# Kernel optimization log

Measured on AMD Instinct MI355X. Metric: run time of the kernel, lower is better.

The kernel has to match this reference:

```python
import jax, jax.numpy as jnp
import numpy as np

D = 512
MOMENTUM = 0.99
NEG_INF = -1.0e9


def setup_inputs() -> dict:
    key = jax.random.key(0)
    ks = jax.random.split(key, 16)
    B, Lq, Lk = 16, 1024, 1024
    s = 0.02
    inp = {
        "uncond_q": jax.random.normal(ks[0], (B, D), jnp.float32),
        "q": jax.random.normal(ks[1], (B, Lq, D), jnp.float32),
        "k": jax.random.normal(ks[2], (B, Lk, D), jnp.float32),
        "v": jax.random.normal(ks[3], (B, Lk, D), jnp.float32),
        "src_key_padding_mask": jax.random.randint(ks[4], (B, Lk), 0, 2) > 0,
        "fallback_score": jnp.zeros((1,), jnp.float32),
        # parameters (torch Linear: y = x @ W.T + b)
        "Wv": jax.random.normal(ks[5], (D, D), jnp.float32) * s,
        "bv": jnp.zeros((D,), jnp.float32),
        "Wf": jax.random.normal(ks[6], (D, D), jnp.float32) * s,
        "bf": jnp.zeros((D,), jnp.float32),
        "W1": jax.random.normal(ks[7], (D, D), jnp.float32) * s,
        "b1": jnp.zeros((D,), jnp.float32),
        "W2": jax.random.normal(ks[8], (D // 2, D), jnp.float32) * s,
        "b2": jnp.zeros((D // 2,), jnp.float32),
        "W3": jax.random.normal(ks[9], (1, D // 2), jnp.float32) * s,
        "b3": jnp.zeros((1,), jnp.float32),
    }
    return inp


def _scorer(x, W1, b1, W2, b2, W3, b3):
    h = jax.nn.relu(x @ W1.T + b1)
    h = jax.nn.relu(h @ W2.T + b2)
    return jnp.tanh(h @ W3.T + b3)


def reference(uncond_q, q, k, v, src_key_padding_mask, fallback_score,
              Wv, bv, Wf, bf, W1, b1, W2, b2, W3, b3):
    B, Lq, _ = q.shape
    v_p = v @ Wv.T + bv                                  # [B,Lk,D]
    default_values = (uncond_q @ Wf.T + bf)[:, None, :]  # [B,1,D]

    scores = jnp.einsum('bqd,bkd->bqk', q, k) / jnp.sqrt(jnp.float32(D))

    # EMA fallback-score update (training mode), detached from grads
    bmax = jax.lax.stop_gradient(scores.max())
    bmin = jax.lax.stop_gradient(scores.min())
    fb = MOMENTUM * fallback_score[0] + (1.0 - MOMENTUM) * (bmax + bmin) / 2.0

    scores = jnp.where(src_key_padding_mask[:, None, :], NEG_INF, scores)
    fb_col = jnp.broadcast_to(fb, (B, Lq, 1))
    scores = jnp.concatenate([scores, fb_col], axis=-1)   # [B,Lq,Lk+1]
    weights = jax.nn.softmax(scores, axis=-1)

    v_padded = jnp.concatenate([v_p, default_values], axis=1)  # [B,Lk+1,D]
    out = jnp.einsum('bqk,bkd->bqd', weights, v_padded)

    return (_scorer(out, W1, b1, W2, b2, W3, b3),
            _scorer(default_values, W1, b1, W2, b2, W3, b3))
```

## Files before the change

### kernel.cpp

```cpp
#include <hip/hip_runtime.h>

typedef _Float16 f16;
typedef f16  f16x8 __attribute__((ext_vector_type(8)));
typedef f16  f16x4 __attribute__((ext_vector_type(4)));
typedef __fp16 fp16x2 __attribute__((ext_vector_type(2)));
typedef float f32x4 __attribute__((ext_vector_type(4)));

__device__ __forceinline__ void gld_lds16(const f16* g, void* l) {
  __builtin_amdgcn_global_load_lds((const __attribute__((address_space(1))) void*)g,
                                   (__attribute__((address_space(3))) void*)l,
                                   16, 0, 0);
}

__device__ __forceinline__ f16x8 pack8(float4 a, float4 b) {
  union { f16x8 v; fp16x2 h[4]; } u;
  u.h[0] = __builtin_amdgcn_cvt_pkrtz(a.x, a.y);
  u.h[1] = __builtin_amdgcn_cvt_pkrtz(a.z, a.w);
  u.h[2] = __builtin_amdgcn_cvt_pkrtz(b.x, b.y);
  u.h[3] = __builtin_amdgcn_cvt_pkrtz(b.z, b.w);
  return u.v;
}

enum { EPI_SCORES = 0, EPI_RELU = 2, EPI_OUT = 3, EPI_BIASR = 4 };

template<int EPI, bool XMAP>
__global__ __launch_bounds__(256)
void gemm_bt(const f16* __restrict__ A, const f16* __restrict__ B, void* __restrict__ C,
             int lda, int ldb, int ldc, int K,
             long long sA, long long sB, long long sC,
             const float* __restrict__ bias, float scale,
             float* __restrict__ mmarr, int nmm,
             const float* __restrict__ wfb, const float* __restrict__ dvv,
             int nx, int nbz)
{
  __shared__ __align__(16) f16 As[4][128][32];
  __shared__ __align__(16) f16 Bs[4][128][32];
  const int tid  = threadIdx.x;
  const int lane = tid & 63;
  const int w    = tid >> 6;
  const int wm   = w >> 1, wn = w & 1;

  const int lin = blockIdx.x;
  int bz, bj;
  if constexpr (XMAP) {
    const int xcd = lin & 7, rest = lin >> 3;
    const int grp = rest / nbz;
    bj = rest - grp * nbz;
    bz = xcd + (grp << 3);
  } else {
    bz = lin / nbz; bj = lin - bz * nbz;
  }
  const int m0 = (bj / nx) * 128, n0 = (bj % nx) * 128;
  const f16* Ab = A + (size_t)bz * sA + (size_t)m0 * lda;
  const f16* Bb = B + (size_t)bz * sB + (size_t)n0 * ldb;

  f32x4 acc[4][4] = {};
  const int nsteps = K >> 5;

#define STAGE(bufb, ks)                                                              \
  {                                                                                  \
    const int k0_ = (ks) << 5;                                                       \
    _Pragma("unroll")                                                                \
    for (int i = 0; i < 2; ++i) {                                                    \
      const int ci = i * 256 + tid;                                                  \
      const int r  = ci >> 2;                                                        \
      const int sg = (ci & 3) ^ ((r >> 1) & 3);                                      \
      gld_lds16(Ab + (size_t)r * lda + k0_ + sg * 8,                                 \
                (char*)As + (bufb) + (size_t)(i * 256 + w * 64) * 16);               \
      gld_lds16(Bb + (size_t)r * ldb + k0_ + sg * 8,                                 \
                (char*)Bs + (bufb) + (size_t)(i * 256 + w * 64) * 16);               \
    }                                                                                \
  }

  STAGE(0, 0)
  if (1 < nsteps) STAGE(8192, 1)
  if (2 < nsteps) STAGE(16384, 2)

  const int elemoff = (((lane >> 4) ^ ((lane >> 1) & 3)) << 3);

  int cur = 0;
  for (int t = 0; t < nsteps; ++t) {
    if (t + 2 < nsteps)      asm volatile("s_waitcnt vmcnt(8)" ::: "memory");
    else if (t + 1 < nsteps) asm volatile("s_waitcnt vmcnt(4)" ::: "memory");
    else                     asm volatile("s_waitcnt vmcnt(0)" ::: "memory");
    __builtin_amdgcn_s_barrier();
    __builtin_amdgcn_sched_barrier(0);
    if (t + 3 < nsteps) STAGE(((cur + 3) & 3) * 8192, t + 3)
    f16x8 af[4], bfr[4];
#pragma unroll
    for (int m = 0; m < 4; ++m)
      af[m] = *(const f16x8*)&As[cur][wm * 64 + m * 16 + (lane & 15)][elemoff];
#pragma unroll
    for (int n = 0; n < 4; ++n)
      bfr[n] = *(const f16x8*)&Bs[cur][wn * 64 + n * 16 + (lane & 15)][elemoff];
    __builtin_amdgcn_s_setprio(1);
#pragma unroll
    for (int m = 0; m < 4; ++m)
#pragma unroll
      for (int n = 0; n < 4; ++n)
        acc[m][n] = __builtin_amdgcn_mfma_f32_16x16x32_f16(af[m], bfr[n], acc[m][n], 0, 0, 0);
    __builtin_amdgcn_s_setprio(0);
    cur = (cur + 1) & 3;
  }
#undef STAGE

  const int col_l = lane & 15;
  const int row_l = (lane >> 4) << 2;

  {
    f16* Ch = (f16*)C + (size_t)bz * sC + (size_t)m0 * ldc + n0;
#pragma unroll
    for (int m = 0; m < 4; ++m)
#pragma unroll
      for (int n = 0; n < 4; ++n)
#pragma unroll
        for (int r = 0; r < 4; ++r) {
          const int rr = wm * 64 + m * 16 + row_l + r;
          const int cc = wn * 64 + n * 16 + col_l;
          float val = acc[m][n][r];
          if constexpr (EPI == EPI_RELU) { val += bias[n0 + cc]; val = fmaxf(val, 0.0f); }
          if constexpr (EPI == EPI_BIASR) val += bias[m0 + rr];
          if constexpr (EPI == EPI_OUT)
            val += wfb[bz * 1024 + m0 + rr] * dvv[bz * 512 + n0 + cc];
          Ch[(size_t)rr * ldc + cc] = (f16)val;
        }
  }
  (void)scale; (void)mmarr; (void)nmm;
}

__global__ __launch_bounds__(512, 2)
void gemm256_scores(const float* __restrict__ A, const float* __restrict__ B, f16* __restrict__ C,
                    float scale, float* __restrict__ mmarr)
{
  __shared__ __align__(16) f16 As[3][256][32];
  __shared__ __align__(16) f16 Bs[3][256][32];
  __shared__ float redm[8], redn[8];
  const int tid  = threadIdx.x;
  const int lane = tid & 63;
  const int w    = tid >> 6;
  const int wm   = w >> 2, wn = w & 3;
  const int lin  = blockIdx.x;
  const int xcd = lin & 7, rest = lin >> 3;
  const int bj  = rest & 15;
  const int bz  = xcd + ((rest >> 4) << 3);
  const int m0 = (bj >> 2) * 256, n0 = (bj & 3) * 256;
  const float* Ab = A + (size_t)bz * 524288 + (size_t)m0 * 512;
  const float* Bb = B + (size_t)bz * 524288 + (size_t)n0 * 512;

  const int r0  = tid >> 2;
  const int sg0 = (tid & 3) ^ ((r0 >> 1) & 3);
  const size_t offG = (size_t)r0 * 512 + sg0 * 8;
  f16* const dstA0 = (f16*)As + (size_t)tid * 8;
  f16* const dstB0 = (f16*)Bs + (size_t)tid * 8;

  f32x4 acc[8][4] = {};

#pragma unroll
  for (int s = 0; s < 2; ++s) {
    const int k0 = s << 5;
    float4 a0 = *(const float4*)(Ab + offG + k0);
    float4 a1 = *(const float4*)(Ab + offG + k0 + 4);
    float4 a2 = *(const float4*)(Ab + offG + k0 + 65536);
    float4 a3 = *(const float4*)(Ab + offG + k0 + 65540);
    float4 b0 = *(const float4*)(Bb + offG + k0);
    float4 b1 = *(const float4*)(Bb + offG + k0 + 4);
    float4 b2 = *(const float4*)(Bb + offG + k0 + 65536);
    float4 b3 = *(const float4*)(Bb + offG + k0 + 65540);
    *(f16x8*)(dstA0 + s * 8192)        = pack8(a0, a1);
    *(f16x8*)(dstA0 + s * 8192 + 4096) = pack8(a2, a3);
    *(f16x8*)(dstB0 + s * 8192)        = pack8(b0, b1);
    *(f16x8*)(dstB0 + s * 8192 + 4096) = pack8(b2, b3);
  }
  __syncthreads();

  const int fr = lane & 15;
  const int elemoff = (((lane >> 4) ^ ((lane >> 1) & 3)) << 3);

  int cur = 0;
  for (int t = 0; t < 16; ++t) {
    float4 a0, a1, a2, a3, b0, b1, b2, b3;
    if (t + 2 < 16) {
      const int k0 = (t + 2) << 5;
      a0 = *(const float4*)(Ab + offG + k0);
      a1 = *(const float4*)(Ab + offG + k0 + 4);
      a2 = *(const float4*)(Ab + offG + k0 + 65536);
      a3 = *(const float4*)(Ab + offG + k0 + 65540);
      b0 = *(const float4*)(Bb + offG + k0);
      b1 = *(const float4*)(Bb + offG + k0 + 4);
      b2 = *(const float4*)(Bb + offG + k0 + 65536);
      b3 = *(const float4*)(Bb + offG + k0 + 65540);
    }
    f16x8 af[8], bfr[4];
#pragma unroll
    for (int m = 0; m < 8; ++m)
      af[m] = *(const f16x8*)&As[cur][wm * 128 + m * 16 + fr][elemoff];
#pragma unroll
    for (int n = 0; n < 4; ++n)
      bfr[n] = *(const f16x8*)&Bs[cur][wn * 64 + n * 16 + fr][elemoff];
    __builtin_amdgcn_s_setprio(1);
#pragma unroll
    for (int m = 0; m < 8; ++m)
#pragma unroll
      for (int n = 0; n < 4; ++n)
        acc[m][n] = __builtin_amdgcn_mfma_f32_16x16x32_f16(af[m], bfr[n], acc[m][n], 0, 0, 0);
    __builtin_amdgcn_s_setprio(0);
    if (t + 2 < 16) {
      int wb = cur + 2; if (wb >= 3) wb -= 3;
      *(f16x8*)(dstA0 + wb * 8192)        = pack8(a0, a1);
      *(f16x8*)(dstA0 + wb * 8192 + 4096) = pack8(a2, a3);
      *(f16x8*)(dstB0 + wb * 8192)        = pack8(b0, b1);
      *(f16x8*)(dstB0 + wb * 8192 + 4096) = pack8(b2, b3);
    }
    __syncthreads();
    cur = (cur + 1 == 3) ? 0 : cur + 1;
  }

  const int col_l = lane & 15;
  const int row_l = (lane >> 4) << 2;
  f16* Ch = C + (size_t)bz * 1048576 + (size_t)m0 * 1024 + n0;
  float lmax = -3.402823466e38f, lmin = 3.402823466e38f;
#pragma unroll
  for (int m = 0; m < 8; ++m)
#pragma unroll
    for (int n = 0; n < 4; ++n)
#pragma unroll
      for (int r = 0; r < 4; ++r) {
        float val = acc[m][n][r] * scale;
        lmax = fmaxf(lmax, val); lmin = fminf(lmin, val);
        Ch[(size_t)(wm * 128 + m * 16 + row_l + r) * 1024 + (wn * 64 + n * 16 + col_l)] = (f16)val;
      }
#pragma unroll
  for (int off = 32; off >= 1; off >>= 1) {
    lmax = fmaxf(lmax, __shfl_xor(lmax, off));
    lmin = fminf(lmin, __shfl_xor(lmin, off));
  }
  if (lane == 0) { redm[w] = lmax; redn[w] = lmin; }
  __syncthreads();
  if (tid == 0) {
    float gm = redm[0], gn = redn[0];
#pragma unroll
    for (int i = 1; i < 8; ++i) { gm = fmaxf(gm, redm[i]); gn = fminf(gn, redn[i]); }
    mmarr[lin] = gm; mmarr[256 + lin] = gn;
  }
}

__global__ __launch_bounds__(256)
void gemm_vpt(const f16* __restrict__ A, const float* __restrict__ B, f16* __restrict__ C,
              const float* __restrict__ bias)
{
  __shared__ __align__(16) f16 As[3][128][32];
  __shared__ __align__(16) f16 Bs[3][128][32];
  const int tid  = threadIdx.x;
  const int lane = tid & 63;
  const int w    = tid >> 6;
  const int wm   = w >> 1, wn = w & 1;
  const int lin  = blockIdx.x;
  const int xcd = lin & 7, rest = lin >> 3;
  const int grp = rest >> 5, bj = rest & 31;
  const int bz  = xcd + (grp << 3);
  const int m0 = (bj >> 3) * 128, n0 = (bj & 7) * 128;
  const f16*   Ab = A + (size_t)m0 * 512;
  const float* Bb = B + (size_t)bz * 524288 + (size_t)n0 * 512;

  const int r0  = tid >> 2;
  const int sg0 = (tid & 3) ^ ((r0 >> 1) & 3);
  const size_t offA = (size_t)r0 * 512 + sg0 * 8;
  const size_t offB = (size_t)r0 * 512 + sg0 * 8;
  f16* const dstA0 = (f16*)As + (size_t)tid * 8;
  f16* const dstB0 = (f16*)Bs + (size_t)tid * 8;

  f32x4 acc[4][4] = {};

#pragma unroll
  for (int s = 0; s < 2; ++s) {
    const int k0 = s << 5;
    f16x8  a0 = *(const f16x8*)(Ab + offA + k0);
    f16x8  a1 = *(const f16x8*)(Ab + offA + k0 + 32768);
    float4 b0 = *(const float4*)(Bb + offB + k0);
    float4 b1 = *(const float4*)(Bb + offB + k0 + 4);
    float4 b2 = *(const float4*)(Bb + offB + k0 + 32768);
    float4 b3 = *(const float4*)(Bb + offB + k0 + 32772);
    *(f16x8*)(dstA0 + s * 4096)        = a0;
    *(f16x8*)(dstA0 + s * 4096 + 2048) = a1;
    *(f16x8*)(dstB0 + s * 4096)        = pack8(b0, b1);
    *(f16x8*)(dstB0 + s * 4096 + 2048) = pack8(b2, b3);
  }
  __syncthreads();

  const int fr = lane & 15;
  const int elemoff = (((lane >> 4) ^ ((lane >> 1) & 3)) << 3);

  int cur = 0;
  for (int t = 0; t < 16; ++t) {
    f16x8  a0, a1; float4 b0, b1, b2, b3;
    if (t + 2 < 16) {
      const int k0 = (t + 2) << 5;
      a0 = *(const f16x8*)(Ab + offA + k0);
      a1 = *(const f16x8*)(Ab + offA + k0 + 32768);
      b0 = *(const float4*)(Bb + offB + k0);
      b1 = *(const float4*)(Bb + offB + k0 + 4);
      b2 = *(const float4*)(Bb + offB + k0 + 32768);
      b3 = *(const float4*)(Bb + offB + k0 + 32772);
    }
    f16x8 af[4], bfr[4];
#pragma unroll
    for (int m = 0; m < 4; ++m)
      af[m] = *(const f16x8*)&As[cur][wm * 64 + m * 16 + fr][elemoff];
#pragma unroll
    for (int n = 0; n < 4; ++n)
      bfr[n] = *(const f16x8*)&Bs[cur][wn * 64 + n * 16 + fr][elemoff];
    __builtin_amdgcn_s_setprio(1);
#pragma unroll
    for (int m = 0; m < 4; ++m)
#pragma unroll
      for (int n = 0; n < 4; ++n)
        acc[m][n] = __builtin_amdgcn_mfma_f32_16x16x32_f16(af[m], bfr[n], acc[m][n], 0, 0, 0);
    __builtin_amdgcn_s_setprio(0);
    if (t + 2 < 16) {
      int wb = cur + 2; if (wb >= 3) wb -= 3;
      *(f16x8*)(dstA0 + wb * 4096)        = a0;
      *(f16x8*)(dstA0 + wb * 4096 + 2048) = a1;
      *(f16x8*)(dstB0 + wb * 4096)        = pack8(b0, b1);
      *(f16x8*)(dstB0 + wb * 4096 + 2048) = pack8(b2, b3);
    }
    __syncthreads();
    cur = (cur + 1 == 3) ? 0 : cur + 1;
  }

  const int col_l = lane & 15;
  const int row_l = (lane >> 4) << 2;
  f16* Ch = C + (size_t)bz * 524288 + (size_t)m0 * 1024 + n0;
#pragma unroll
  for (int m = 0; m < 4; ++m)
#pragma unroll
    for (int n = 0; n < 4; ++n)
#pragma unroll
      for (int r = 0; r < 4; ++r) {
        const int rr = wm * 64 + m * 16 + row_l + r;
        const int cc = wn * 64 + n * 16 + col_l;
        Ch[(size_t)rr * 1024 + cc] = (f16)(acc[m][n][r] + bias[m0 + rr]);
      }
}

__global__ __launch_bounds__(256)
void reduce_mm(const float* __restrict__ mmarr, int n,
               const float* __restrict__ fallback, float* __restrict__ fbv,
               const unsigned char* __restrict__ mask, unsigned* __restrict__ mm)
{
  __shared__ float rm[4], rn[4];
  __shared__ int redc[256];
  const int lane = threadIdx.x & 63, w = threadIdx.x >> 6;
  float mx = -3.402823466e38f, mn = 3.402823466e38f;
  for (int i = threadIdx.x; i < n; i += 256) {
    mx = fmaxf(mx, mmarr[i]);
    mn = fminf(mn, mmarr[n + i]);
  }
#pragma unroll
  for (int off = 32; off >= 1; off >>= 1) {
    mx = fmaxf(mx, __shfl_xor(mx, off));
    mn = fminf(mn, __shfl_xor(mn, off));
  }
  if (lane == 0) { rm[w] = mx; rn[w] = mn; }
  int c = 0;
  for (int i = threadIdx.x; i < 16384; i += 256) c += (mask[i] != 0) ? 1 : 0;
  redc[threadIdx.x] = c;
  __syncthreads();
  for (int s = 128; s > 0; s >>= 1) {
    if (threadIdx.x < s) redc[threadIdx.x] += redc[threadIdx.x + s];
    __syncthreads();
  }
  if (threadIdx.x == 0) {
    float gmax = fmaxf(fmaxf(rm[0], rm[1]), fmaxf(rm[2], rm[3]));
    float gmin = fminf(fminf(rn[0], rn[1]), fminf(rn[2], rn[3]));
    fbv[0] = 0.99f * fallback[0] + 0.005f * (gmax + gmin);
    mm[0] = (unsigned)redc[0];
  }
}

__global__ __launch_bounds__(256)
void front_k(const float* __restrict__ wv, const float* __restrict__ w1,
             const float* __restrict__ w2,
             f16* __restrict__ owv, f16* __restrict__ ow1, f16* __restrict__ ow2,
             const float* __restrict__ uq, const float* __restrict__ Wf,
             const float* __restrict__ bfv, float* __restrict__ dv)
{
  const int blk = blockIdx.x;
  if (blk < 640) {
    int i = blk * 256 + threadIdx.x;
    const float* src; f16* dst; int j;
    if (i < 65536)       { src = wv; dst = owv; j = i; }
    else if (i < 131072) { src = w1; dst = ow1; j = i - 65536; }
    else                 { src = w2; dst = ow2; j = i - 131072; }
    float4 x = *(const float4*)(src + (size_t)j * 4);
    f16x4 o = { (f16)x.x, (f16)x.y, (f16)x.z, (f16)x.w };
    *(f16x4*)(dst + (size_t)j * 4) = o;
  } else {
    const int gw   = ((blk - 640) * 256 + threadIdx.x) >> 6;
    const int lane = threadIdx.x & 63;
    const int b = gw >> 9, j = gw & 511;
    const float* x  = uq + (size_t)b * 512;
    const float* wr = Wf + (size_t)j * 512;
    const int o = lane * 8;
    float4 x0 = *(const float4*)(x + o),  x1 = *(const float4*)(x + o + 4);
    float4 w0 = *(const float4*)(wr + o), w1v = *(const float4*)(wr + o + 4);
    float s = x0.x*w0.x + x0.y*w0.y + x0.z*w0.z + x0.w*w0.w
            + x1.x*w1v.x + x1.y*w1v.y + x1.z*w1v.z + x1.w*w1v.w;
#pragma unroll
    for (int off = 32; off >= 1; off >>= 1) s += __shfl_xor(s, off);
    if (lane == 0) dv[gw] = s + bfv[j];
  }
}

__global__ __launch_bounds__(256)
void softmax_rows(const f16* __restrict__ scores, const void* __restrict__ maskp,
                  const float* __restrict__ fbv, const unsigned* __restrict__ mm,
                  f16* __restrict__ Wt, float* __restrict__ wfb)
{
  __shared__ float red[8];
  const int row  = blockIdx.x;
  const int b    = row >> 10;
  const int tid  = threadIdx.x;
  const int lane = tid & 63, w = tid >> 6;
  const float fb = fbv[0];
  const unsigned mode = (mm[0] > 5000u) ? 1u : 0u;
  const f16* s = scores + (size_t)row * 1024;
  const int k0 = tid * 4;
  f16x4 sv = *(const f16x4*)(s + k0);
  float x[4];
  if (mode) {
    const unsigned char* m8 = (const unsigned char*)maskp + b * 1024 + k0;
    x[0] = m8[0] ? -1e9f : (float)sv[0];  x[1] = m8[1] ? -1e9f : (float)sv[1];
    x[2] = m8[2] ? -1e9f : (float)sv[2];  x[3] = m8[3] ? -1e9f : (float)sv[3];
  } else {
    const int* mi = (const int*)maskp + b * 1024 + k0;
    x[0] = mi[0] ? -1e9f : (float)sv[0];  x[1] = mi[1] ? -1e9f : (float)sv[1];
    x[2] = mi[2] ? -1e9f : (float)sv[2];  x[3] = mi[3] ? -1e9f : (float)sv[3];
  }
  float mx = fmaxf(fmaxf(x[0], x[1]), fmaxf(x[2], x[3]));
#pragma unroll
  for (int off = 32; off >= 1; off >>= 1) mx = fmaxf(mx, __shfl_xor(mx, off));
  if (lane == 0) red[w] = mx;
  __syncthreads();
  mx = fmaxf(fmaxf(fmaxf(red[0], red[1]), fmaxf(red[2], red[3])), fb);
  float e0 = expf(x[0] - mx), e1 = expf(x[1] - mx), e2 = expf(x[2] - mx), e3 = expf(x[3] - mx);
  float sum = (e0 + e1) + (e2 + e3);
#pragma unroll
  for (int off = 32; off >= 1; off >>= 1) sum += __shfl_xor(sum, off);
  if (lane == 0) red[4 + w] = sum;
  __syncthreads();
  float efb = expf(fb - mx);
  float Z = ((red[4] + red[5]) + (red[6] + red[7])) + efb;
  float inv = 1.0f / Z;
  f16x4 o = { (f16)(e0 * inv), (f16)(e1 * inv), (f16)(e2 * inv), (f16)(e3 * inv) };
  *(f16x4*)&Wt[(size_t)row * 1024 + k0] = o;
  if (tid == 0) wfb[row] = efb * inv;
}

template<int IN, int ACT>
__global__ __launch_bounds__(256)
void fc_wave(const float* __restrict__ X, const float* __restrict__ W,
             const float* __restrict__ bias, float* __restrict__ Y, int OutN)
{
  const int gw   = (blockIdx.x * 256 + threadIdx.x) >> 6;
  const int lane = threadIdx.x & 63;
  const int b = gw / OutN, j = gw - b * OutN;
  const float* x  = X + (size_t)b * IN;
  const float* wr = W + (size_t)j * IN;
  float s = 0.f;
  if constexpr (IN == 512) {
    const int o = lane * 8;
    float4 x0 = *(const float4*)(x + o),  x1 = *(const float4*)(x + o + 4);
    float4 w0 = *(const float4*)(wr + o), w1 = *(const float4*)(wr + o + 4);
    s = x0.x*w0.x + x0.y*w0.y + x0.z*w0.z + x0.w*w0.w
      + x1.x*w1.x + x1.y*w1.y + x1.z*w1.z + x1.w*w1.w;
  } else {
    const int o = lane * 4;
    float4 x0 = *(const float4*)(x + o);
    float4 w0 = *(const float4*)(wr + o);
    s = x0.x*w0.x + x0.y*w0.y + x0.z*w0.z + x0.w*w0.w;
  }
#pragma unroll
  for (int off = 32; off >= 1; off >>= 1) s += __shfl_xor(s, off);
  if (lane == 0) {
    float val = s + bias[ACT == 2 ? 0 : j];
    if constexpr (ACT == 1) val = fmaxf(val, 0.f);
    if constexpr (ACT == 2) val = tanhf(val);
    Y[gw] = val;
  }
}

__global__ __launch_bounds__(256)
void y_kernel(const f16* __restrict__ h2, const float* __restrict__ W3,
              const float* __restrict__ b3, float* __restrict__ outp)
{
  int row = blockIdx.x * 16 + (threadIdx.x >> 4);
  int l   = threadIdx.x & 15;
  const f16* h = h2 + (size_t)row * 256 + l * 16;
  float s = 0.f;
#pragma unroll
  for (int j = 0; j < 16; ++j) s += (float)h[j] * W3[l * 16 + j];
#pragma unroll
  for (int off = 1; off < 16; off <<= 1) s += __shfl_xor(s, off);
  if (l == 0) outp[row] = tanhf(s + b3[0]);
}

extern "C" void kernel_launch(void* const* d_in, const int* in_sizes, int n_in,
                              void* d_out, int out_size, void* d_ws, size_t ws_size,
                              hipStream_t stream) {
  const float* uq       = (const float*)d_in[0];
  const float* q        = (const float*)d_in[1];
  const float* kk       = (const float*)d_in[2];
  const float* v        = (const float*)d_in[3];
  const void*  mask     = d_in[4];
  const float* fallback = (const float*)d_in[5];
  const float* Wv = (const float*)d_in[6];
  const float* bv = (const float*)d_in[7];
  const float* Wf = (const float*)d_in[8];
  const float* bf = (const float*)d_in[9];
  const float* W1 = (const float*)d_in[10];
  const float* b1 = (const float*)d_in[11];
  const float* W2 = (const float*)d_in[12];
  const float* b2 = (const float*)d_in[13];
  const float* W3 = (const float*)d_in[14];
  const float* b3 = (const float*)d_in[15];
  float* outp = (float*)d_out;

  char* ws = (char*)d_ws;
  const size_t MB = 1ull << 20;
  f16*  scores = (f16*)ws;
  f16*  h1b  = (f16*)ws;
  f16*  h2b  = (f16*)(ws + 16 * MB);
  f16*  vpt  = (f16*)(ws + 32 * MB);
  f16*  outb = (f16*)(ws + 48 * MB);
  f16*  wts  = (f16*)(ws + 64 * MB);
  char* cst  = ws + 112 * MB;
  f16*  Wv16 = (f16*)(cst);
  f16*  W116 = (f16*)(cst + 512 * 1024);
  f16*  W216 = (f16*)(cst + 1024 * 1024);
  float* dv   = (float*)(cst + 1280 * 1024);
  float* wfb  = (float*)(cst + 1312 * 1024);
  float* h1d  = (float*)(cst + 1376 * 1024);
  float* h2d  = (float*)(cst + 1408 * 1024);
  unsigned* mm = (unsigned*)(cst + 1424 * 1024);
  float* fbv   = (float*)(cst + 1428 * 1024);
  float* mmarr = (float*)(cst + 1432 * 1024);

  front_k<<<2688, 256, 0, stream>>>(Wv, W1, W2, Wv16, W116, W216,
                                    uq, Wf, bf, dv);

  gemm256_scores<<<256, 512, 0, stream>>>(q, kk, scores, 0.04419417382415922f, mmarr);

  reduce_mm<<<1, 256, 0, stream>>>(mmarr, 256, fallback, fbv,
                                   (const unsigned char*)mask, mm);

  softmax_rows<<<16384, 256, 0, stream>>>(scores, mask, fbv, mm, wts, wfb);

  gemm_vpt<<<512, 256, 0, stream>>>(Wv16, v, vpt, bv);

  gemm_bt<EPI_OUT, true><<<512, 256, 0, stream>>>(
      wts, vpt, outb, 1024, 1024, 512, 1024,
      1048576LL, 524288LL, 524288LL,
      nullptr, 1.f, nullptr, 0, wfb, dv, 4, 32);

  gemm_bt<EPI_RELU, false><<<512, 256, 0, stream>>>(
      outb, W116, h1b, 512, 512, 512, 512, 0LL, 0LL, 0LL,
      b1, 1.f, nullptr, 0, nullptr, nullptr, 4, 512);

  gemm_bt<EPI_RELU, false><<<256, 256, 0, stream>>>(
      h1b, W216, h2b, 512, 512, 256, 512, 0LL, 0LL, 0LL,
      b2, 1.f, nullptr, 0, nullptr, nullptr, 2, 256);

  y_kernel<<<1024, 256, 0, stream>>>(h2b, W3, b3, outp);

  fc_wave<512, 1><<<2048, 256, 0, stream>>>(dv, W1, b1, h1d, 512);
  fc_wave<512, 1><<<1024, 256, 0, stream>>>(h1d, W2, b2, h2d, 256);
  fc_wave<256, 2><<<4, 256, 0, stream>>>(h2d, W3, b3, outp + 16384, 1);

  (void)in_sizes; (void)n_in; (void)out_size; (void)ws_size;
}
```

Measured before the change: 161.2 us.

## Fuse softmax and V projection into one launch, fold reductions into existing kernels

Merges the row softmax and the V-projection GEMM into a single heterogeneous kernel whose block index selects which role to play. The global min/max reduction is recomputed redundantly in every softmax block, and the mask count moves into an extra block of the front kernel, so the single-block reduce_mm launch goes away. The aim is to cut two kernel launches and serial gaps, and to let the GEMM blocks overlap with softmax blocks. In exchange each softmax block now reads 512 floats and does extra reductions and barriers. The shared-memory footprint becomes the larger GEMM size for all blocks, which may reduce softmax occupancy.

```diff
diff --git a/kernel.cpp b/kernel.cpp
--- a/kernel.cpp
+++ b/kernel.cpp
@@ -29,7 +29,6 @@
              int lda, int ldb, int ldc, int K,
              long long sA, long long sB, long long sC,
              const float* __restrict__ bias, float scale,
-             float* __restrict__ mmarr, int nmm,
              const float* __restrict__ wfb, const float* __restrict__ dvv,
              int nx, int nbz)
 {
@@ -125,7 +124,7 @@
           Ch[(size_t)rr * ldc + cc] = (f16)val;
         }
   }
-  (void)scale; (void)mmarr; (void)nmm;
+  (void)scale;
 }
 
 __global__ __launch_bounds__(512, 2)
@@ -245,135 +244,158 @@
 }
 
 __global__ __launch_bounds__(256)
-void gemm_vpt(const f16* __restrict__ A, const float* __restrict__ B, f16* __restrict__ C,
-              const float* __restrict__ bias)
+void smvp(const f16* __restrict__ scores, const void* __restrict__ maskp,
+          const float* __restrict__ fallback, const float* __restrict__ mmarr,
+          const unsigned* __restrict__ mm,
+          f16* __restrict__ Wt, float* __restrict__ wfb,
+          const f16* __restrict__ Wv16, const float* __restrict__ v,
+          f16* __restrict__ vpt, const float* __restrict__ bv)
 {
-  __shared__ __align__(16) f16 As[3][128][32];
-  __shared__ __align__(16) f16 Bs[3][128][32];
+  __shared__ __align__(16) char smem[49152];
+  const int blk  = blockIdx.x;
   const int tid  = threadIdx.x;
   const int lane = tid & 63;
   const int w    = tid >> 6;
-  const int wm   = w >> 1, wn = w & 1;
-  const int lin  = blockIdx.x;
-  const int xcd = lin & 7, rest = lin >> 3;
-  const int grp = rest >> 5, bj = rest & 31;
-  const int bz  = xcd + (grp << 3);
-  const int m0 = (bj >> 3) * 128, n0 = (bj & 7) * 128;
-  const f16*   Ab = A + (size_t)m0 * 512;
-  const float* Bb = B + (size_t)bz * 524288 + (size_t)n0 * 512;
-
-  const int r0  = tid >> 2;
-  const int sg0 = (tid & 3) ^ ((r0 >> 1) & 3);
-  const size_t offA = (size_t)r0 * 512 + sg0 * 8;
-  const size_t offB = (size_t)r0 * 512 + sg0 * 8;
-  f16* const dstA0 = (f16*)As + (size_t)tid * 8;
-  f16* const dstB0 = (f16*)Bs + (size_t)tid * 8;
-
-  f32x4 acc[4][4] = {};
-
-#pragma unroll
-  for (int s = 0; s < 2; ++s) {
-    const int k0 = s << 5;
-    f16x8  a0 = *(const f16x8*)(Ab + offA + k0);
-    f16x8  a1 = *(const f16x8*)(Ab + offA + k0 + 32768);
-    float4 b0 = *(const float4*)(Bb + offB + k0);
-    float4 b1 = *(const float4*)(Bb + offB + k0 + 4);
-    float4 b2 = *(const float4*)(Bb + offB + k0 + 32768);
-    float4 b3 = *(const float4*)(Bb + offB + k0 + 32772);
-    *(f16x8*)(dstA0 + s * 4096)        = a0;
-    *(f16x8*)(dstA0 + s * 4096 + 2048) = a1;
-    *(f16x8*)(dstB0 + s * 4096)        = pack8(b0, b1);
-    *(f16x8*)(dstB0 + s * 4096 + 2048) = pack8(b2, b3);
-  }
-  __syncthreads();
-
-  const int fr = lane & 15;
-  const int elemoff = (((lane >> 4) ^ ((lane >> 1) & 3)) << 3);
-
-  int cur = 0;
-  for (int t = 0; t < 16; ++t) {
-    f16x8  a0, a1; float4 b0, b1, b2, b3;
-    if (t + 2 < 16) {
-      const int k0 = (t + 2) << 5;
-      a0 = *(const f16x8*)(Ab + offA + k0);
-      a1 = *(const f16x8*)(Ab + offA + k0 + 32768);
-      b0 = *(const float4*)(Bb + offB + k0);
-      b1 = *(const float4*)(Bb + offB + k0 + 4);
-      b2 = *(const float4*)(Bb + offB + k0 + 32768);
-      b3 = *(const float4*)(Bb + offB + k0 + 32772);
-    }
-    f16x8 af[4], bfr[4];
+
+  if (blk < 16384) {
+    float* red = (float*)smem;
+    float mx0 = mmarr[tid];
+    float mn0 = mmarr[256 + tid];
+#pragma unroll
+    for (int off = 32; off >= 1; off >>= 1) {
+      mx0 = fmaxf(mx0, __shfl_xor(mx0, off));
+      mn0 = fminf(mn0, __shfl_xor(mn0, off));
+    }
+    if (lane == 0) { red[w] = mx0; red[4 + w] = mn0; }
+    __syncthreads();
+    const float gmax = fmaxf(fmaxf(red[0], red[1]), fmaxf(red[2], red[3]));
+    const float gmin = fminf(fminf(red[4], red[5]), fminf(red[6], red[7]));
+    const float fb = 0.99f * fallback[0] + 0.005f * (gmax + gmin);
+    const unsigned mode = (mm[0] > 5000u) ? 1u : 0u;
+    __syncthreads();
+    const int row = blk;
+    const int b   = row >> 10;
+    const f16* s = scores + (size_t)row * 1024;
+    const int k0 = tid * 4;
+    f16x4 sv = *(const f16x4*)(s + k0);
+    float x[4];
+    if (mode) {
+      const unsigned char* m8 = (const unsigned char*)maskp + b * 1024 + k0;
+      x[0] = m8[0] ? -1e9f : (float)sv[0];  x[1] = m8[1] ? -1e9f : (float)sv[1];
+      x[2] = m8[2] ? -1e9f : (float)sv[2];  x[3] = m8[3] ? -1e9f : (float)sv[3];
+    } else {
+      const int* mi = (const int*)maskp + b * 1024 + k0;
+      x[0] = mi[0] ? -1e9f : (float)sv[0];  x[1] = mi[1] ? -1e9f : (float)sv[1];
+      x[2] = mi[2] ? -1e9f : (float)sv[2];  x[3] = mi[3] ? -1e9f : (float)sv[3];
+    }
+    float mx = fmaxf(fmaxf(x[0], x[1]), fmaxf(x[2], x[3]));
+#pragma unroll
+    for (int off = 32; off >= 1; off >>= 1) mx = fmaxf(mx, __shfl_xor(mx, off));
+    if (lane == 0) red[w] = mx;
+    __syncthreads();
+    mx = fmaxf(fmaxf(fmaxf(red[0], red[1]), fmaxf(red[2], red[3])), fb);
+    float e0 = expf(x[0] - mx), e1 = expf(x[1] - mx), e2 = expf(x[2] - mx), e3 = expf(x[3] - mx);
+    float sum = (e0 + e1) + (e2 + e3);
+#pragma unroll
+    for (int off = 32; off >= 1; off >>= 1) sum += __shfl_xor(sum, off);
+    if (lane == 0) red[4 + w] = sum;
+    __syncthreads();
+    float efb = expf(fb - mx);
+    float Z = ((red[4] + red[5]) + (red[6] + red[7])) + efb;
+    float inv = 1.0f / Z;
+    f16x4 o = { (f16)(e0 * inv), (f16)(e1 * inv), (f16)(e2 * inv), (f16)(e3 * inv) };
+    *(f16x4*)&Wt[(size_t)row * 1024 + k0] = o;
+    if (tid == 0) wfb[row] = efb * inv;
+  } else {
+    f16* const AsB = (f16*)smem;
+    f16* const BsB = AsB + 12288;
+    const int wm = w >> 1, wn = w & 1;
+    const int lin  = blk - 16384;
+    const int xcd = lin & 7, rest = lin >> 3;
+    const int grp = rest >> 5, bj = rest & 31;
+    const int bz  = xcd + (grp << 3);
+    const int m0 = (bj >> 3) * 128, n0 = (bj & 7) * 128;
+    const f16*   Ab = Wv16 + (size_t)m0 * 512;
+    const float* Bb = v + (size_t)bz * 524288 + (size_t)n0 * 512;
+
+    const int r0  = tid >> 2;
+    const int sg0 = (tid & 3) ^ ((r0 >> 1) & 3);
+    const size_t offA = (size_t)r0 * 512 + sg0 * 8;
+    const size_t offB = (size_t)r0 * 512 + sg0 * 8;
+    f16* const dstA0 = AsB + (size_t)tid * 8;
+    f16* const dstB0 = BsB + (size_t)tid * 8;
+
+    f32x4 acc[4][4] = {};
+
+#pragma unroll
+    for (int s = 0; s < 2; ++s) {
+      const int k0 = s << 5;
+      f16x8  a0 = *(const f16x8*)(Ab + offA + k0);
+      f16x8  a1 = *(const f16x8*)(Ab + offA + k0 + 32768);
+      float4 b0 = *(const float4*)(Bb + offB + k0);
+      float4 b1 = *(const float4*)(Bb + offB + k0 + 4);
+      float4 b2 = *(const float4*)(Bb + offB + k0 + 32768);
+      float4 b3 = *(const float4*)(Bb + offB + k0 + 32772);
+      *(f16x8*)(dstA0 + s * 4096)        = a0;
+      *(f16x8*)(dstA0 + s * 4096 + 2048) = a1;
+      *(f16x8*)(dstB0 + s * 4096)        = pack8(b0, b1);
+      *(f16x8*)(dstB0 + s * 4096 + 2048) = pack8(b2, b3);
+    }
+    __syncthreads();
+
+    const int fr = lane & 15;
+    const int elemoff = (((lane >> 4) ^ ((lane >> 1) & 3)) << 3);
+
+    int cur = 0;
+    for (int t = 0; t < 16; ++t) {
+      f16x8  a0, a1; float4 b0, b1, b2, b3;
+      if (t + 2 < 16) {
+        const int k0 = (t + 2) << 5;
+        a0 = *(const f16x8*)(Ab + offA + k0);
+        a1 = *(const f16x8*)(Ab + offA + k0 + 32768);
+        b0 = *(const float4*)(Bb + offB + k0);
+        b1 = *(const float4*)(Bb + offB + k0 + 4);
+        b2 = *(const float4*)(Bb + offB + k0 + 32768);
+        b3 = *(const float4*)(Bb + offB + k0 + 32772);
+      }
+      f16x8 af[4], bfr[4];
+#pragma unroll
+      for (int m = 0; m < 4; ++m)
+        af[m] = *(const f16x8*)(AsB + cur * 4096 + (wm * 64 + m * 16 + fr) * 32 + elemoff);
+#pragma unroll
+      for (int n = 0; n < 4; ++n)
+        bfr[n] = *(const f16x8*)(BsB + cur * 4096 + (wn * 64 + n * 16 + fr) * 32 + elemoff);
+      __builtin_amdgcn_s_setprio(1);
+#pragma unroll
+      for (int m = 0; m < 4; ++m)
+#pragma unroll
+        for (int n = 0; n < 4; ++n)
+          acc[m][n] = __builtin_amdgcn_mfma_f32_16x16x32_f16(af[m], bfr[n], acc[m][n], 0, 0, 0);
+      __builtin_amdgcn_s_setprio(0);
+      if (t + 2 < 16) {
+        int wb = cur + 2; if (wb >= 3) wb -= 3;
+        *(f16x8*)(dstA0 + wb * 4096)        = a0;
+        *(f16x8*)(dstA0 + wb * 4096 + 2048) = a1;
+        *(f16x8*)(dstB0 + wb * 4096)        = pack8(b0, b1);
+        *(f16x8*)(dstB0 + wb * 4096 + 2048) = pack8(b2, b3);
+      }
+      __syncthreads();
+      cur = (cur + 1 == 3) ? 0 : cur + 1;
+    }
+
+    const int col_l = lane & 15;
+    const int row_l = (lane >> 4) << 2;
+    f16* Ch = vpt + (size_t)bz * 524288 + (size_t)m0 * 1024 + n0;
 #pragma unroll
     for (int m = 0; m < 4; ++m)
-      af[m] = *(const f16x8*)&As[cur][wm * 64 + m * 16 + fr][elemoff];
-#pragma unroll
-    for (int n = 0; n < 4; ++n)
-      bfr[n] = *(const f16x8*)&Bs[cur][wn * 64 + n * 16 + fr][elemoff];
-    __builtin_amdgcn_s_setprio(1);
-#pragma unroll
-    for (int m = 0; m < 4; ++m)
 #pragma unroll
       for (int n = 0; n < 4; ++n)
-        acc[m][n] = __builtin_amdgcn_mfma_f32_16x16x32_f16(af[m], bfr[n], acc[m][n], 0, 0, 0);
-    __builtin_amdgcn_s_setprio(0);
-    if (t + 2 < 16) {
-      int wb = cur + 2; if (wb >= 3) wb -= 3;
-      *(f16x8*)(dstA0 + wb * 4096)        = a0;
-      *(f16x8*)(dstA0 + wb * 4096 + 2048) = a1;
-      *(f16x8*)(dstB0 + wb * 4096)        = pack8(b0, b1);
-      *(f16x8*)(dstB0 + wb * 4096 + 2048) = pack8(b2, b3);
-    }
-    __syncthreads();
-    cur = (cur + 1 == 3) ? 0 : cur + 1;
-  }
-
-  const int col_l = lane & 15;
-  const int row_l = (lane >> 4) << 2;
-  f16* Ch = C + (size_t)bz * 524288 + (size_t)m0 * 1024 + n0;
-#pragma unroll
-  for (int m = 0; m < 4; ++m)
-#pragma unroll
-    for (int n = 0; n < 4; ++n)
-#pragma unroll
-      for (int r = 0; r < 4; ++r) {
-        const int rr = wm * 64 + m * 16 + row_l + r;
-        const int cc = wn * 64 + n * 16 + col_l;
-        Ch[(size_t)rr * 1024 + cc] = (f16)(acc[m][n][r] + bias[m0 + rr]);
-      }
-}
-
-__global__ __launch_bounds__(256)
-void reduce_mm(const float* __restrict__ mmarr, int n,
-               const float* __restrict__ fallback, float* __restrict__ fbv,
-               const unsigned char* __restrict__ mask, unsigned* __restrict__ mm)
-{
-  __shared__ float rm[4], rn[4];
-  __shared__ int redc[256];
-  const int lane = threadIdx.x & 63, w = threadIdx.x >> 6;
-  float mx = -3.402823466e38f, mn = 3.402823466e38f;
-  for (int i = threadIdx.x; i < n; i += 256) {
-    mx = fmaxf(mx, mmarr[i]);
-    mn = fminf(mn, mmarr[n + i]);
-  }
-#pragma unroll
-  for (int off = 32; off >= 1; off >>= 1) {
-    mx = fmaxf(mx, __shfl_xor(mx, off));
-    mn = fminf(mn, __shfl_xor(mn, off));
-  }
-  if (lane == 0) { rm[w] = mx; rn[w] = mn; }
-  int c = 0;
-  for (int i = threadIdx.x; i < 16384; i += 256) c += (mask[i] != 0) ? 1 : 0;
-  redc[threadIdx.x] = c;
-  __syncthreads();
-  for (int s = 128; s > 0; s >>= 1) {
-    if (threadIdx.x < s) redc[threadIdx.x] += redc[threadIdx.x + s];
-    __syncthreads();
-  }
-  if (threadIdx.x == 0) {
-    float gmax = fmaxf(fmaxf(rm[0], rm[1]), fmaxf(rm[2], rm[3]));
-    float gmin = fminf(fminf(rn[0], rn[1]), fminf(rn[2], rn[3]));
-    fbv[0] = 0.99f * fallback[0] + 0.005f * (gmax + gmin);
-    mm[0] = (unsigned)redc[0];
+#pragma unroll
+        for (int r = 0; r < 4; ++r) {
+          const int rr = wm * 64 + m * 16 + row_l + r;
+          const int cc = wn * 64 + n * 16 + col_l;
+          Ch[(size_t)rr * 1024 + cc] = (f16)(acc[m][n][r] + bv[m0 + rr]);
+        }
   }
 }
 
@@ -382,7 +404,8 @@
              const float* __restrict__ w2,
              f16* __restrict__ owv, f16* __restrict__ ow1, f16* __restrict__ ow2,
              const float* __restrict__ uq, const float* __restrict__ Wf,
-             const float* __restrict__ bfv, float* __restrict__ dv)
+             const float* __restrict__ bfv, float* __restrict__ dv,
+             const unsigned char* __restrict__ mask, unsigned* __restrict__ mm)
 {
   const int blk = blockIdx.x;
   if (blk < 640) {
@@ -394,7 +417,7 @@
     float4 x = *(const float4*)(src + (size_t)j * 4);
     f16x4 o = { (f16)x.x, (f16)x.y, (f16)x.z, (f16)x.w };
     *(f16x4*)(dst + (size_t)j * 4) = o;
-  } else {
+  } else if (blk < 2688) {
     const int gw   = ((blk - 640) * 256 + threadIdx.x) >> 6;
     const int lane = threadIdx.x & 63;
     const int b = gw >> 9, j = gw & 511;
@@ -408,52 +431,18 @@
 #pragma unroll
     for (int off = 32; off >= 1; off >>= 1) s += __shfl_xor(s, off);
     if (lane == 0) dv[gw] = s + bfv[j];
-  }
-}
-
-__global__ __launch_bounds__(256)
-void softmax_rows(const f16* __restrict__ scores, const void* __restrict__ maskp,
-                  const float* __restrict__ fbv, const unsigned* __restrict__ mm,
-                  f16* __restrict__ Wt, float* __restrict__ wfb)
-{
-  __shared__ float red[8];
-  const int row  = blockIdx.x;
-  const int b    = row >> 10;
-  const int tid  = threadIdx.x;
-  const int lane = tid & 63, w = tid >> 6;
-  const float fb = fbv[0];
-  const unsigned mode = (mm[0] > 5000u) ? 1u : 0u;
-  const f16* s = scores + (size_t)row * 1024;
-  const int k0 = tid * 4;
-  f16x4 sv = *(const f16x4*)(s + k0);
-  float x[4];
-  if (mode) {
-    const unsigned char* m8 = (const unsigned char*)maskp + b * 1024 + k0;
-    x[0] = m8[0] ? -1e9f : (float)sv[0];  x[1] = m8[1] ? -1e9f : (float)sv[1];
-    x[2] = m8[2] ? -1e9f : (float)sv[2];  x[3] = m8[3] ? -1e9f : (float)sv[3];
   } else {
-    const int* mi = (const int*)maskp + b * 1024 + k0;
-    x[0] = mi[0] ? -1e9f : (float)sv[0];  x[1] = mi[1] ? -1e9f : (float)sv[1];
-    x[2] = mi[2] ? -1e9f : (float)sv[2];  x[3] = mi[3] ? -1e9f : (float)sv[3];
-  }
-  float mx = fmaxf(fmaxf(x[0], x[1]), fmaxf(x[2], x[3]));
-#pragma unroll
-  for (int off = 32; off >= 1; off >>= 1) mx = fmaxf(mx, __shfl_xor(mx, off));
-  if (lane == 0) red[w] = mx;
-  __syncthreads();
-  mx = fmaxf(fmaxf(fmaxf(red[0], red[1]), fmaxf(red[2], red[3])), fb);
-  float e0 = expf(x[0] - mx), e1 = expf(x[1] - mx), e2 = expf(x[2] - mx), e3 = expf(x[3] - mx);
-  float sum = (e0 + e1) + (e2 + e3);
-#pragma unroll
-  for (int off = 32; off >= 1; off >>= 1) sum += __shfl_xor(sum, off);
-  if (lane == 0) red[4 + w] = sum;
-  __syncthreads();
-  float efb = expf(fb - mx);
-  float Z = ((red[4] + red[5]) + (red[6] + red[7])) + efb;
-  float inv = 1.0f / Z;
-  f16x4 o = { (f16)(e0 * inv), (f16)(e1 * inv), (f16)(e2 * inv), (f16)(e3 * inv) };
-  *(f16x4*)&Wt[(size_t)row * 1024 + k0] = o;
-  if (tid == 0) wfb[row] = efb * inv;
+    __shared__ int redc[256];
+    int c = 0;
+    for (int i = threadIdx.x; i < 16384; i += 256) c += (mask[i] != 0) ? 1 : 0;
+    redc[threadIdx.x] = c;
+    __syncthreads();
+    for (int s = 128; s > 0; s >>= 1) {
+      if (threadIdx.x < s) redc[threadIdx.x] += redc[threadIdx.x + s];
+      __syncthreads();
+    }
+    if (threadIdx.x == 0) mm[0] = (unsigned)redc[0];
+  }
 }
 
 template<int IN, int ACT>
@@ -542,33 +531,29 @@
   float* h1d  = (float*)(cst + 1376 * 1024);
   float* h2d  = (float*)(cst + 1408 * 1024);
   unsigned* mm = (unsigned*)(cst + 1424 * 1024);
-  float* fbv   = (float*)(cst + 1428 * 1024);
   float* mmarr = (float*)(cst + 1432 * 1024);
 
-  front_k<<<2688, 256, 0, stream>>>(Wv, W1, W2, Wv16, W116, W216,
-                                    uq, Wf, bf, dv);
+  front_k<<<2689, 256, 0, stream>>>(Wv, W1, W2, Wv16, W116, W216,
+                                    uq, Wf, bf, dv,
+                                    (const unsigned char*)mask, mm);
 
   gemm256_scores<<<256, 512, 0, stream>>>(q, kk, scores, 0.04419417382415922f, mmarr);
 
-  reduce_mm<<<1, 256, 0, stream>>>(mmarr, 256, fallback, fbv,
-                                   (const unsigned char*)mask, mm);
-
-  softmax_rows<<<16384, 256, 0, stream>>>(scores, mask, fbv, mm, wts, wfb);
-
-  gemm_vpt<<<512, 256, 0, stream>>>(Wv16, v, vpt, bv);
+  smvp<<<16896, 256, 0, stream>>>(scores, mask, fallback, mmarr, mm,
+                                  wts, wfb, Wv16, v, vpt, bv);
 
   gemm_bt<EPI_OUT, true><<<512, 256, 0, stream>>>(
       wts, vpt, outb, 1024, 1024, 512, 1024,
       1048576LL, 524288LL, 524288LL,
-      nullptr, 1.f, nullptr, 0, wfb, dv, 4, 32);
+      nullptr, 1.f, wfb, dv, 4, 32);
 
   gemm_bt<EPI_RELU, false><<<512, 256, 0, stream>>>(
       outb, W116, h1b, 512, 512, 512, 512, 0LL, 0LL, 0LL,
-      b1, 1.f, nullptr, 0, nullptr, nullptr, 4, 512);
+      b1, 1.f, nullptr, nullptr, 4, 512);
 
   gemm_bt<EPI_RELU, false><<<256, 256, 0, stream>>>(
       h1b, W216, h2b, 512, 512, 256, 512, 0LL, 0LL, 0LL,
-      b2, 1.f, nullptr, 0, nullptr, nullptr, 2, 256);
+      b2, 1.f, nullptr, nullptr, 2, 256);
 
   y_kernel<<<1024, 256, 0, stream>>>(h2b, W3, b3, outp);
 
```

Result: slower. 195.5 us (+21.3%).
